# Kernel optimization log

Hardware: AMD Instinct MI355X
Metric: run time of the kernel (lower is better)

The kernel has to match this reference:

```python
import jax, jax.numpy as jnp
import numpy as np

POOL = 7          # cfg.POOLING_SIZE
STRIDE = 16.0     # cfg.RPN_ANCHOR_STRIDE (y and x)


def _bilinear_sample(fm, py, px):
    """grid_sample (bilinear, zero padding, align_corners=True) for one image.
    fm: [C,H,W]; py, px: [R,Ho,Wo] pixel-space coords. Returns [C,R,Ho,Wo]."""
    C, H, W = fm.shape
    x0 = jnp.floor(px); y0 = jnp.floor(py)
    x1 = x0 + 1.0;      y1 = y0 + 1.0
    wx1 = px - x0; wx0 = 1.0 - wx1
    wy1 = py - y0; wy0 = 1.0 - wy1
    fm_flat = fm.reshape(C, H * W)

    def gather(y, x):
        valid = (x >= 0) & (x <= W - 1) & (y >= 0) & (y <= H - 1)
        xi = jnp.clip(x, 0, W - 1).astype(jnp.int32)
        yi = jnp.clip(y, 0, H - 1).astype(jnp.int32)
        v = jnp.take(fm_flat, (yi * W + xi).reshape(-1), axis=1)
        return v.reshape((C,) + y.shape) * valid.astype(fm.dtype)

    return (gather(y0, x0) * (wy0 * wx0) + gather(y0, x1) * (wy0 * wx1)
          + gather(y1, x0) * (wy1 * wx0) + gather(y1, x1) * (wy1 * wx1))


def setup_inputs() -> dict:
    key = jax.random.key(0)
    k1, k2, k3 = jax.random.split(key, 3)
    N, R, C, H, W = 4, 256, 1024, 50, 50
    # boxes (y, x, h, w) in original image coords (800x800 image, stride 16)
    yx = jax.random.uniform(k1, (N, R, 2), jnp.float32, 0.0, 600.0)
    hw = jax.random.uniform(k2, (N, R, 2), jnp.float32, 32.0, 200.0)
    rois = jnp.concatenate([yx, hw], axis=-1)
    feature_map = jax.random.normal(k3, (N, C, H, W), jnp.float32)
    return {"rois": rois, "feature_map": feature_map}


def reference(rois, feature_map):
    N, C, H, W = feature_map.shape
    R = rois.shape[1]
    y1 = rois[:, :, 0] / STRIDE
    x1 = rois[:, :, 1] / STRIDE
    y2 = (rois[:, :, 0] + rois[:, :, 2]) / STRIDE
    x2 = (rois[:, :, 1] + rois[:, :, 3]) / STRIDE
    # affine theta (align_corners=True convention, matching the (W-1) formulas)
    a  = (x2 - x1) / (W - 1)
    tx = (x1 + x2 - W + 1) / (W - 1)
    b  = (y2 - y1) / (H - 1)
    ty = (y1 + y2 - H + 1) / (H - 1)
    Ho = Wo = POOL * 2
    gx = jnp.linspace(-1.0, 1.0, Wo).astype(rois.dtype)
    gy = jnp.linspace(-1.0, 1.0, Ho).astype(rois.dtype)
    xs = a[:, :, None, None] * gx[None, None, None, :] + tx[:, :, None, None]  # [N,R,1,Wo]
    ys = b[:, :, None, None] * gy[None, None, :, None] + ty[:, :, None, None]  # [N,R,Ho,1]
    # normalized -> pixel coords (align_corners=True)
    px = jnp.broadcast_to((xs + 1.0) * (W - 1) / 2.0, (N, R, Ho, Wo))
    py = jnp.broadcast_to((ys + 1.0) * (H - 1) / 2.0, (N, R, Ho, Wo))
    sampled = jax.vmap(_bilinear_sample)(feature_map, py, px)  # [N,C,R,Ho,Wo]
    crops = jnp.transpose(sampled, (0, 2, 1, 3, 4))            # [N,R,C,Ho,Wo]
    crops = crops.reshape(N, R, C, POOL, 2, POOL, 2).max(axis=(4, 6))
    return crops  # [N,R,C,7,7]
```

## Files before the change

kernel.cpp:

```cpp
#include <hip/hip_runtime.h>
#include <math.h>

static constexpr int N_ = 4, R_ = 256, C_ = 1024, H_ = 50, W_ = 50, P_ = 7;
static constexpr int HW_ = H_ * W_;
static constexpr int PP_ = P_ * P_;
static constexpr int CHB_ = 4;
static constexpr int WVS_ = 8;
static constexpr int P4_ = 2502;
static constexpr int NTASK = R_ * PP_;
static constexpr int NIT = NTASK / 64;

__device__ __forceinline__ void axis_w(float p0, float p1, int L,
                                       int& i0c, float wA[2], float wB[3]) {
    float f0 = floorf(p0); int i0 = (int)f0; float a0 = p0 - f0;
    float f1 = floorf(p1); int i1 = (int)f1; float a1 = p1 - f1;
    const bool o = (i1 > i0);
    wA[0] = 1.0f - a0; wA[1] = a0;
    wB[0] = o ? 0.0f : (1.0f - a1);
    wB[1] = o ? (1.0f - a1) : a1;
    wB[2] = o ? a1 : 0.0f;
    if (i0 > L - 1)     { wA[0] = 0.0f; wB[0] = 0.0f; }
    if (i0 + 1 > L - 1) { wA[1] = 0.0f; wB[1] = 0.0f; }
    if (i0 + 2 > L - 1) {               wB[2] = 0.0f; }
    i0c = min(max(i0, 0), L - 1);
}

__global__ __launch_bounds__(512, 8) void roipool_kernel(
    const float* __restrict__ rois,
    const float* __restrict__ fm,
    float* __restrict__ out) {

    __shared__ float4 sh4[P4_];

    const int b  = blockIdx.x;
    const int n  = b >> 8;
    const int c0 = (b & 255) * CHB_;
    const int tid = threadIdx.x;
    const int lane = tid & 63;
    const int wv = __builtin_amdgcn_readfirstlane(tid >> 6);

    {
        const int gpb = (n * C_ + c0) * HW_;
        for (int p = tid; p < P4_; p += 512) {
            const int sp = min(p, HW_ - 1);
            float4 v;
            v.x = fm[gpb + sp];
            v.y = fm[gpb + HW_ + sp];
            v.z = fm[gpb + 2 * HW_ + sp];
            v.w = fm[gpb + 3 * HW_ + sp];
            sh4[p] = v;
        }
    }
    __syncthreads();

    const float4* __restrict__ rois4 = reinterpret_cast<const float4*>(rois) + n * R_;
    const size_t obase = ((size_t)n * R_ * C_ + c0) * PP_;

    {
        const int t0 = (wv << 6) | lane;
        int ri = (int)((unsigned)t0 / 49u);
        int px = t0 - ri * 49;

        for (int it = wv; it < NIT; it += WVS_) {
            const int pi = (int)((unsigned)px / 7u);
            const int pj = px - pi * 7;

            const float4 roi = rois4[ri];
            const float y1 = roi.x * 0.0625f;
            const float x1 = roi.y * 0.0625f;
            const float y2 = (roi.x + roi.z) * 0.0625f;
            const float x2 = (roi.y + roi.w) * 0.0625f;
            const float sy = (y2 - y1) * (1.0f / 13.0f);
            const float sx = (x2 - x1) * (1.0f / 13.0f);

            const float py0 = y1 + sy * (float)(2 * pi);
            const float py1 = y1 + sy * (float)(2 * pi + 1);
            const float qx0 = x1 + sx * (float)(2 * pj);
            const float qx1 = x1 + sx * (float)(2 * pj + 1);

            int iy0; float wyA[2], wyB[3];
            axis_w(py0, py1, H_, iy0, wyA, wyB);
            int ix0; float wxA[2], wxB[3];
            axis_w(qx0, qx1, W_, ix0, wxA, wxB);

            const float4* __restrict__ B0 = sh4 + (iy0 * W_ + ix0);
            const float4* __restrict__ B1 = sh4 + (min(iy0 + 1, H_ - 1) * W_ + ix0);
            const float4* __restrict__ B2 = sh4 + (min(iy0 + 2, H_ - 1) * W_ + ix0);

            const float4 v00 = B0[0], v01 = B0[1], v02 = B0[2];
            const float4 v10 = B1[0], v11 = B1[1], v12 = B1[2];
            const float4 v20 = B2[0], v21 = B2[1], v22 = B2[2];

            float r0, r1, r2, r3;
#define REDUCE_CH(CMP, RES) do {                                               \
        const float tA0 = fmaf(wyA[1], v10.CMP, wyA[0] * v00.CMP);             \
        const float tA1 = fmaf(wyA[1], v11.CMP, wyA[0] * v01.CMP);             \
        const float tA2 = fmaf(wyA[1], v12.CMP, wyA[0] * v02.CMP);             \
        const float tB0 = fmaf(wyB[2], v20.CMP, fmaf(wyB[1], v10.CMP, wyB[0] * v00.CMP)); \
        const float tB1 = fmaf(wyB[2], v21.CMP, fmaf(wyB[1], v11.CMP, wyB[0] * v01.CMP)); \
        const float tB2 = fmaf(wyB[2], v22.CMP, fmaf(wyB[1], v12.CMP, wyB[0] * v02.CMP)); \
        const float s00 = fmaf(wxA[1], tA1, wxA[0] * tA0);                     \
        const float s01 = fmaf(wxB[2], tA2, fmaf(wxB[1], tA1, wxB[0] * tA0));  \
        const float s10 = fmaf(wxA[1], tB1, wxA[0] * tB0);                     \
        const float s11 = fmaf(wxB[2], tB2, fmaf(wxB[1], tB1, wxB[0] * tB0));  \
        RES = fmaxf(fmaxf(s00, s01), fmaxf(s10, s11));                         \
    } while (0)
            REDUCE_CH(x, r0);
            REDUCE_CH(y, r1);
            REDUCE_CH(z, r2);
            REDUCE_CH(w, r3);
#undef REDUCE_CH

            float* __restrict__ po = out + obase + (size_t)ri * C_ * PP_ + px;
            po[0]       = r0;
            po[PP_]     = r1;
            po[2 * PP_] = r2;
            po[3 * PP_] = r3;

            px += 22; ri += 10;
            if (px >= 49) { px -= 49; ri += 1; }
        }
    }
}

extern "C" void kernel_launch(void* const* d_in, const int* in_sizes, int n_in,
                              void* d_out, int out_size, void* d_ws, size_t ws_size,
                              hipStream_t stream) {
    const float* rois = (const float*)d_in[0];
    const float* fm   = (const float*)d_in[1];
    float* out        = (float*)d_out;

    const int blocks = N_ * (C_ / CHB_);
    roipool_kernel<<<blocks, 512, 0, stream>>>(rois, fm, out);
}
```

Before: 68.25 us.

## Precompute per-task sampling geometry table in separate kernel and load it

Adds a small pre-pass kernel that computes, for every (image, roi, pooled cell) task, the packed shared-memory base index, row offsets, output offset and the bilinear weights, and writes them to the workspace as 48-byte entries. The main kernel now reads these entries instead of recomputing the ROI geometry, floors and weight selection in each of the 256 channel-group blocks per image. This removes redundant ALU work but adds a second launch and about 2.4 MB of table reads per image across blocks, which should mostly hit in L2.

Measured after the change: 67.73 us, median of 3. No clear change (-0.8%).

```diff
diff --git a/kernel.cpp b/kernel.cpp
--- a/kernel.cpp
+++ b/kernel.cpp
@@ -9,6 +9,7 @@
 static constexpr int P4_ = 2502;
 static constexpr int NTASK = R_ * PP_;
 static constexpr int NIT = NTASK / 64;
+static constexpr int TBE_ = 3;
 
 __device__ __forceinline__ void axis_w(float p0, float p1, int L,
                                        int& i0c, float wA[2], float wB[3]) {
@@ -25,8 +26,50 @@
     i0c = min(max(i0, 0), L - 1);
 }
 
+__global__ __launch_bounds__(256) void geom_kernel(
+    const float* __restrict__ rois, uint* __restrict__ tab) {
+    const int g = blockIdx.x * 256 + threadIdx.x;
+    const int n  = (int)((unsigned)g / (unsigned)NTASK);
+    const int t  = g - n * NTASK;
+    const int ri = (int)((unsigned)t / 49u);
+    const int px = t - ri * 49;
+    const int pi = (int)((unsigned)px / 7u);
+    const int pj = px - pi * 7;
+
+    const float4 roi = reinterpret_cast<const float4*>(rois)[n * R_ + ri];
+    const float y1 = roi.x * 0.0625f;
+    const float x1 = roi.y * 0.0625f;
+    const float y2 = (roi.x + roi.z) * 0.0625f;
+    const float x2 = (roi.y + roi.w) * 0.0625f;
+    const float sy = (y2 - y1) * (1.0f / 13.0f);
+    const float sx = (x2 - x1) * (1.0f / 13.0f);
+
+    const float py0 = y1 + sy * (float)(2 * pi);
+    const float py1 = y1 + sy * (float)(2 * pi + 1);
+    const float qx0 = x1 + sx * (float)(2 * pj);
+    const float qx1 = x1 + sx * (float)(2 * pj + 1);
+
+    int iy0; float wyA[2], wyB[3];
+    axis_w(py0, py1, H_, iy0, wyA, wyB);
+    int ix0; float wxA[2], wxB[3];
+    axis_w(qx0, qx1, W_, ix0, wxA, wxB);
+
+    const int b0 = iy0 * W_ + ix0;
+    const int d1 = min(iy0 + 1, H_ - 1) - iy0;
+    const int d2 = min(iy0 + 2, H_ - 1) - iy0;
+    const uint packed = (uint)b0 | ((uint)d1 << 12) | ((uint)d2 << 14);
+    const uint oo = (uint)(ri * (C_ * PP_) + px);
+
+    uint4* e = reinterpret_cast<uint4*>(tab) + (size_t)g * TBE_;
+    e[0] = make_uint4(packed, oo, __float_as_uint(wyA[0]), __float_as_uint(wyA[1]));
+    e[1] = make_uint4(__float_as_uint(wyB[0]), __float_as_uint(wyB[1]),
+                      __float_as_uint(wyB[2]), __float_as_uint(wxA[0]));
+    e[2] = make_uint4(__float_as_uint(wxA[1]), __float_as_uint(wxB[0]),
+                      __float_as_uint(wxB[1]), __float_as_uint(wxB[2]));
+}
+
 __global__ __launch_bounds__(512, 8) void roipool_kernel(
-    const float* __restrict__ rois,
+    const uint* __restrict__ tab,
     const float* __restrict__ fm,
     float* __restrict__ out) {
 
@@ -53,73 +96,60 @@
     }
     __syncthreads();
 
-    const float4* __restrict__ rois4 = reinterpret_cast<const float4*>(rois) + n * R_;
     const size_t obase = ((size_t)n * R_ * C_ + c0) * PP_;
+    const uint4* __restrict__ tb =
+        reinterpret_cast<const uint4*>(tab) + (size_t)(n * NTASK + lane) * TBE_;
 
-    {
-        const int t0 = (wv << 6) | lane;
-        int ri = (int)((unsigned)t0 / 49u);
-        int px = t0 - ri * 49;
+    for (int it = wv; it < NIT; it += WVS_) {
+        const uint4* __restrict__ e = tb + (size_t)(it << 6) * TBE_;
+        const uint4 E0 = e[0];
+        const uint4 E1 = e[1];
+        const uint4 E2 = e[2];
 
-        for (int it = wv; it < NIT; it += WVS_) {
-            const int pi = (int)((unsigned)px / 7u);
-            const int pj = px - pi * 7;
+        const int b0 = (int)(E0.x & 0xFFFu);
+        const int b1 = b0 + (int)((E0.x >> 12) & 3u) * W_;
+        const int b2 = b0 + (int)((E0.x >> 14) & 3u) * W_;
 
-            const float4 roi = rois4[ri];
-            const float y1 = roi.x * 0.0625f;
-            const float x1 = roi.y * 0.0625f;
-            const float y2 = (roi.x + roi.z) * 0.0625f;
-            const float x2 = (roi.y + roi.w) * 0.0625f;
-            const float sy = (y2 - y1) * (1.0f / 13.0f);
-            const float sx = (x2 - x1) * (1.0f / 13.0f);
+        const float wyA0 = __uint_as_float(E0.z), wyA1 = __uint_as_float(E0.w);
+        const float wyB0 = __uint_as_float(E1.x), wyB1 = __uint_as_float(E1.y);
+        const float wyB2 = __uint_as_float(E1.z);
+        const float wxA0 = __uint_as_float(E1.w), wxA1 = __uint_as_float(E2.x);
+        const float wxB0 = __uint_as_float(E2.y), wxB1 = __uint_as_float(E2.z);
+        const float wxB2 = __uint_as_float(E2.w);
 
-            const float py0 = y1 + sy * (float)(2 * pi);
-            const float py1 = y1 + sy * (float)(2 * pi + 1);
-            const float qx0 = x1 + sx * (float)(2 * pj);
-            const float qx1 = x1 + sx * (float)(2 * pj + 1);
+        const float4* __restrict__ B0 = sh4 + b0;
+        const float4* __restrict__ B1 = sh4 + b1;
+        const float4* __restrict__ B2 = sh4 + b2;
 
-            int iy0; float wyA[2], wyB[3];
-            axis_w(py0, py1, H_, iy0, wyA, wyB);
-            int ix0; float wxA[2], wxB[3];
-            axis_w(qx0, qx1, W_, ix0, wxA, wxB);
+        const float4 v00 = B0[0], v01 = B0[1], v02 = B0[2];
+        const float4 v10 = B1[0], v11 = B1[1], v12 = B1[2];
+        const float4 v20 = B2[0], v21 = B2[1], v22 = B2[2];
 
-            const float4* __restrict__ B0 = sh4 + (iy0 * W_ + ix0);
-            const float4* __restrict__ B1 = sh4 + (min(iy0 + 1, H_ - 1) * W_ + ix0);
-            const float4* __restrict__ B2 = sh4 + (min(iy0 + 2, H_ - 1) * W_ + ix0);
-
-            const float4 v00 = B0[0], v01 = B0[1], v02 = B0[2];
-            const float4 v10 = B1[0], v11 = B1[1], v12 = B1[2];
-            const float4 v20 = B2[0], v21 = B2[1], v22 = B2[2];
-
-            float r0, r1, r2, r3;
+        float r0, r1, r2, r3;
 #define REDUCE_CH(CMP, RES) do {                                               \
-        const float tA0 = fmaf(wyA[1], v10.CMP, wyA[0] * v00.CMP);             \
-        const float tA1 = fmaf(wyA[1], v11.CMP, wyA[0] * v01.CMP);             \
-        const float tA2 = fmaf(wyA[1], v12.CMP, wyA[0] * v02.CMP);             \
-        const float tB0 = fmaf(wyB[2], v20.CMP, fmaf(wyB[1], v10.CMP, wyB[0] * v00.CMP)); \
-        const float tB1 = fmaf(wyB[2], v21.CMP, fmaf(wyB[1], v11.CMP, wyB[0] * v01.CMP)); \
-        const float tB2 = fmaf(wyB[2], v22.CMP, fmaf(wyB[1], v12.CMP, wyB[0] * v02.CMP)); \
-        const float s00 = fmaf(wxA[1], tA1, wxA[0] * tA0);                     \
-        const float s01 = fmaf(wxB[2], tA2, fmaf(wxB[1], tA1, wxB[0] * tA0));  \
-        const float s10 = fmaf(wxA[1], tB1, wxA[0] * tB0);                     \
-        const float s11 = fmaf(wxB[2], tB2, fmaf(wxB[1], tB1, wxB[0] * tB0));  \
+        const float tA0 = fmaf(wyA1, v10.CMP, wyA0 * v00.CMP);                 \
+        const float tA1 = fmaf(wyA1, v11.CMP, wyA0 * v01.CMP);                 \
+        const float tA2 = fmaf(wyA1, v12.CMP, wyA0 * v02.CMP);                 \
+        const float tB0 = fmaf(wyB2, v20.CMP, fmaf(wyB1, v10.CMP, wyB0 * v00.CMP)); \
+        const float tB1 = fmaf(wyB2, v21.CMP, fmaf(wyB1, v11.CMP, wyB0 * v01.CMP)); \
+        const float tB2 = fmaf(wyB2, v22.CMP, fmaf(wyB1, v12.CMP, wyB0 * v02.CMP)); \
+        const float s00 = fmaf(wxA1, tA1, wxA0 * tA0);                         \
+        const float s01 = fmaf(wxB2, tA2, fmaf(wxB1, tA1, wxB0 * tA0));        \
+        const float s10 = fmaf(wxA1, tB1, wxA0 * tB0);                         \
+        const float s11 = fmaf(wxB2, tB2, fmaf(wxB1, tB1, wxB0 * tB0));        \
         RES = fmaxf(fmaxf(s00, s01), fmaxf(s10, s11));                         \
     } while (0)
-            REDUCE_CH(x, r0);
-            REDUCE_CH(y, r1);
-            REDUCE_CH(z, r2);
-            REDUCE_CH(w, r3);
+        REDUCE_CH(x, r0);
+        REDUCE_CH(y, r1);
+        REDUCE_CH(z, r2);
+        REDUCE_CH(w, r3);
 #undef REDUCE_CH
 
-            float* __restrict__ po = out + obase + (size_t)ri * C_ * PP_ + px;
-            po[0]       = r0;
-            po[PP_]     = r1;
-            po[2 * PP_] = r2;
-            po[3 * PP_] = r3;
-
-            px += 22; ri += 10;
-            if (px >= 49) { px -= 49; ri += 1; }
-        }
+        float* __restrict__ po = out + obase + E0.y;
+        po[0]       = r0;
+        po[PP_]     = r1;
+        po[2 * PP_] = r2;
+        po[3 * PP_] = r3;
     }
 }
 
@@ -129,7 +159,9 @@
     const float* rois = (const float*)d_in[0];
     const float* fm   = (const float*)d_in[1];
     float* out        = (float*)d_out;
+    uint* tab         = (uint*)d_ws;
 
+    geom_kernel<<<196, 256, 0, stream>>>(rois, tab);
     const int blocks = N_ * (C_ / CHB_);
-    roipool_kernel<<<blocks, 512, 0, stream>>>(rois, fm, out);
+    roipool_kernel<<<blocks, 512, 0, stream>>>(tab, fm, out);
 }
```
